# Kernel tuning notes

Hardware: AMD Instinct MI355X
Metric: run time of the kernel (lower is better)

Reference implementation:

```python
import jax, jax.numpy as jnp
import numpy as np

B, N_IN, N = 8, 256, 8192
D, K = 64, 512


def setup_inputs() -> dict:
    key = jax.random.key(0)
    k1, k2, k3 = jax.random.split(key, 3)
    z = jax.random.normal(k1, (B, N_IN, N), dtype=jnp.float32)
    W = jax.random.normal(k2, (D, N_IN), dtype=jnp.float32) * (1.0 / np.sqrt(N_IN))
    emb = jax.random.normal(k3, (K, D), dtype=jnp.float32)
    ind_hist = jnp.zeros((K,), dtype=jnp.float32)
    return {"z": z, "W": W, "emb": emb, "ind_hist": ind_hist}


def reference(z, W, emb, ind_hist):
    # 1x1 Conv1d, no bias: (B, n_in, N) x (d, n_in) -> (B, d, N)
    ze = jnp.einsum('bin,di->bdn', z, W)
    emb_sg = jax.lax.stop_gradient(emb)  # StopGrad on codebook

    # Squared L2 distance ze[b,:,n] vs emb[k,:], expanded identity to avoid (B,K,d,N)
    ze_sq = jnp.sum(ze * ze, axis=1)                      # (B, N)
    emb_sq = jnp.sum(emb_sg * emb_sg, axis=1)             # (K,)
    cross = jnp.einsum('bdn,kd->bkn', ze, emb_sg)         # (B, K, N)
    l2norm_sq = ze_sq[:, None, :] + emb_sq[None, :, None] - 2.0 * cross  # (B, K, N)

    ind = jnp.argmin(l2norm_sq, axis=1)                   # (B, N) nearest code per timestep
    zq = jnp.take(emb_sg, ind, axis=0).transpose(0, 2, 1)  # (B, d, N)

    # ReplaceGrad straight-through: forward value zq, gradient routed to ze
    zq_rg = ze + jax.lax.stop_gradient(zq - ze)

    # Scatter histogram of chosen indices, accumulated into ind_hist buffer
    counts = jax.ops.segment_sum(
        jnp.ones((B * N,), dtype=ind_hist.dtype), ind.reshape(-1), num_segments=K)
    new_hist = ind_hist + counts

    return zq_rg, new_hist
```

## Files before the change

### kernel.cpp

```cpp
#include <hip/hip_runtime.h>

#define B_SZ   8
#define NIN    256
#define NCOL   8192
#define DDIM   64
#define KCODES 512
#define ZQ_ELEMS (8ull * 64ull * 8192ull)

__global__ __launch_bounds__(256) void vq_prep(const float* __restrict__ W,
                                               const float* __restrict__ emb,
                                               const float* __restrict__ ind_hist,
                                               float* __restrict__ Wt,
                                               float* __restrict__ emb_sq,
                                               float* __restrict__ hist_out)
{
    int t = blockIdx.x * 256 + threadIdx.x;
    if (t < NIN * DDIM) {
        int i = t >> 6;
        int d = t & 63;
        Wt[t] = W[d * NIN + i];
    }
    if (t < KCODES) {
        const float* __restrict__ ek = emb + t * DDIM;
        float s = 0.f;
        #pragma unroll
        for (int d = 0; d < DDIM; ++d) s = fmaf(ek[d], ek[d], s);
        emb_sq[t] = s;
        hist_out[t] = ind_hist[t];
    }
}

__global__ __launch_bounds__(256, 4) void vq_main(const float* __restrict__ z,
                                                  const float* __restrict__ Wt,
                                                  const float* __restrict__ emb,
                                                  const float* __restrict__ emb_sq,
                                                  float* __restrict__ out,
                                                  float* __restrict__ hist)
{
    __shared__ float ze_lds[64][DDIM + 4];
    __shared__ float bw_lds[4][64];
    __shared__ int   bk_lds[4][64];

    const int tid = threadIdx.x;
    const int cl  = tid & 63;
    const int w   = __builtin_amdgcn_readfirstlane(tid >> 6);
    const int C   = blockIdx.x * 64 + cl;
    const int b   = C >> 13;
    const int n   = C & (NCOL - 1);

    {
        const float* __restrict__ zp = z + (size_t)b * NIN * NCOL + n;
        const float* __restrict__ wp = Wt + w * 16;

        float acc[16];
        #pragma unroll
        for (int j = 0; j < 16; ++j) acc[j] = 0.f;

        for (int i = 0; i < NIN; i += 2) {
            float z0 = zp[(size_t)(i + 0) * NCOL];
            float z1 = zp[(size_t)(i + 1) * NCOL];
            const float* __restrict__ w0 = wp + (size_t)i * DDIM;
            const float* __restrict__ w1 = w0 + DDIM;
            #pragma unroll
            for (int j = 0; j < 16; ++j) {
                float a = acc[j];
                a = fmaf(w0[j], z0, a);
                a = fmaf(w1[j], z1, a);
                acc[j] = a;
            }
        }
        #pragma unroll
        for (int j = 0; j < 16; ++j) ze_lds[cl][w * 16 + j] = acc[j];
    }
    __syncthreads();

    float ze[DDIM];
    #pragma unroll
    for (int j = 0; j < DDIM / 4; ++j) {
        float4 v = *reinterpret_cast<const float4*>(&ze_lds[cl][4 * j]);
        ze[4 * j + 0] = v.x;
        ze[4 * j + 1] = v.y;
        ze[4 * j + 2] = v.z;
        ze[4 * j + 3] = v.w;
    }

    float zesq = 0.f;
    #pragma unroll
    for (int d = 0; d < DDIM; ++d) zesq = fmaf(ze[d], ze[d], zesq);

    float best = 3.4e38f;
    int bestk = KCODES * w / 4;
    const int k0 = w * (KCODES / 4);
    for (int kk = 0; kk < KCODES / 4; ++kk) {
        const int k = k0 + kk;
        const float* __restrict__ ek = emb + (size_t)k * DDIM;
        float cr = 0.f;
        #pragma unroll
        for (int d = 0; d < DDIM; ++d) cr = fmaf(ek[d], ze[d], cr);
        float dist = (zesq + emb_sq[k]) - 2.0f * cr;
        if (dist < best) { best = dist; bestk = k; }
    }
    bw_lds[w][cl] = best;
    bk_lds[w][cl] = bestk;
    __syncthreads();

    float fb = bw_lds[0][cl];
    int   fk = bk_lds[0][cl];
    #pragma unroll
    for (int ww = 1; ww < 4; ++ww) {
        float v = bw_lds[ww][cl];
        int   kv = bk_lds[ww][cl];
        if (v < fb) { fb = v; fk = kv; }
    }

    if (w == 0) atomicAdd(hist + fk, 1.0f);

    const float4* __restrict__ eb =
        reinterpret_cast<const float4*>(emb + (size_t)fk * DDIM) + w * 4;
    float* __restrict__ op = out + ((size_t)b * DDIM + w * 16) * NCOL + n;
    #pragma unroll
    for (int v = 0; v < 4; ++v) {
        float4 e = eb[v];
        float z0 = ze_lds[cl][w * 16 + 4 * v + 0];
        float z1 = ze_lds[cl][w * 16 + 4 * v + 1];
        float z2 = ze_lds[cl][w * 16 + 4 * v + 2];
        float z3 = ze_lds[cl][w * 16 + 4 * v + 3];
        op[(size_t)(4 * v + 0) * NCOL] = z0 + (e.x - z0);
        op[(size_t)(4 * v + 1) * NCOL] = z1 + (e.y - z1);
        op[(size_t)(4 * v + 2) * NCOL] = z2 + (e.z - z2);
        op[(size_t)(4 * v + 3) * NCOL] = z3 + (e.w - z3);
    }
}

extern "C" void kernel_launch(void* const* d_in, const int* in_sizes, int n_in,
                              void* d_out, int out_size, void* d_ws, size_t ws_size,
                              hipStream_t stream)
{
    const float* z        = (const float*)d_in[0];
    const float* W        = (const float*)d_in[1];
    const float* emb      = (const float*)d_in[2];
    const float* ind_hist = (const float*)d_in[3];

    float* out  = (float*)d_out;
    float* hist = out + ZQ_ELEMS;

    float* Wt     = (float*)d_ws;
    float* emb_sq = Wt + NIN * DDIM;

    hipLaunchKernelGGL(vq_prep, dim3(64), dim3(256), 0, stream,
                       W, emb, ind_hist, Wt, emb_sq, hist);

    hipLaunchKernelGGL(vq_main, dim3(1024), dim3(256), 0, stream,
                       z, Wt, emb, emb_sq, out, hist);
}
```

Baseline: 134.2 us.

## Split fused VQ kernel into conv, split-K search, and finalize kernels

Splits the single fused kernel into three stages. The 1x1 conv writes ze to the output buffer. A codebook search runs on twice as many blocks, each covering half the codes, and merges results with 64-bit packed atomicMin on per-column candidates. A final kernel reads ze back, gathers the chosen code and updates the histogram. The aim is more parallelism and occupancy for the search, at the cost of extra global round-trips of ze, extra launches and atomics. The conv loop is also unrolled by 4 instead of 2.

```diff
diff --git a/kernel.cpp b/kernel.cpp
--- a/kernel.cpp
+++ b/kernel.cpp
@@ -1,10 +1,10 @@
 #include <hip/hip_runtime.h>
 
-#define B_SZ   8
 #define NIN    256
 #define NCOL   8192
 #define DDIM   64
 #define KCODES 512
+#define NCTOT  65536
 #define ZQ_ELEMS (8ull * 64ull * 8192ull)
 
 __global__ __launch_bounds__(256) void vq_prep(const float* __restrict__ W,
@@ -12,9 +12,11 @@
                                                const float* __restrict__ ind_hist,
                                                float* __restrict__ Wt,
                                                float* __restrict__ emb_sq,
+                                               unsigned long long* __restrict__ cand,
                                                float* __restrict__ hist_out)
 {
     int t = blockIdx.x * 256 + threadIdx.x;
+    cand[t] = ~0ull;
     if (t < NIN * DDIM) {
         int i = t >> 6;
         int d = t & 63;
@@ -30,17 +32,10 @@
     }
 }
 
-__global__ __launch_bounds__(256, 4) void vq_main(const float* __restrict__ z,
+__global__ __launch_bounds__(256, 4) void vq_conv(const float* __restrict__ z,
                                                   const float* __restrict__ Wt,
-                                                  const float* __restrict__ emb,
-                                                  const float* __restrict__ emb_sq,
-                                                  float* __restrict__ out,
-                                                  float* __restrict__ hist)
-{
-    __shared__ float ze_lds[64][DDIM + 4];
-    __shared__ float bw_lds[4][64];
-    __shared__ int   bk_lds[4][64];
-
+                                                  float* __restrict__ out)
+{
     const int tid = threadIdx.x;
     const int cl  = tid & 63;
     const int w   = __builtin_amdgcn_readfirstlane(tid >> 6);
@@ -48,50 +43,88 @@
     const int b   = C >> 13;
     const int n   = C & (NCOL - 1);
 
+    const float* __restrict__ zp = z + (size_t)b * NIN * NCOL + n;
+    const float* __restrict__ wp = Wt + w * 16;
+
+    float acc[16];
+    #pragma unroll
+    for (int j = 0; j < 16; ++j) acc[j] = 0.f;
+
+    for (int i = 0; i < NIN; i += 4) {
+        float z0 = zp[(size_t)(i + 0) * NCOL];
+        float z1 = zp[(size_t)(i + 1) * NCOL];
+        float z2 = zp[(size_t)(i + 2) * NCOL];
+        float z3 = zp[(size_t)(i + 3) * NCOL];
+        const float* __restrict__ w0 = wp + (size_t)(i + 0) * DDIM;
+        const float* __restrict__ w1 = wp + (size_t)(i + 1) * DDIM;
+        const float* __restrict__ w2 = wp + (size_t)(i + 2) * DDIM;
+        const float* __restrict__ w3 = wp + (size_t)(i + 3) * DDIM;
+        #pragma unroll
+        for (int j = 0; j < 16; ++j) {
+            float a = acc[j];
+            a = fmaf(w0[j], z0, a);
+            a = fmaf(w1[j], z1, a);
+            a = fmaf(w2[j], z2, a);
+            a = fmaf(w3[j], z3, a);
+            acc[j] = a;
+        }
+    }
+
+    float* __restrict__ op = out + ((size_t)b * DDIM + w * 16) * NCOL + n;
+    #pragma unroll
+    for (int j = 0; j < 16; ++j) op[(size_t)j * NCOL] = acc[j];
+}
+
+__global__ __launch_bounds__(256) void vq_search(const float* __restrict__ zeb,
+                                                 const float* __restrict__ emb,
+                                                 const float* __restrict__ emb_sq,
+                                                 unsigned long long* __restrict__ cand)
+{
+    __shared__ float ze_lds[64][DDIM + 4];
+
+    const int tid   = threadIdx.x;
+    const int C0    = (blockIdx.x >> 1) * 64;
+    const int khalf = blockIdx.x & 1;
+    const int b     = C0 >> 13;
+    const int n0    = C0 & (NCOL - 1);
+
     {
-        const float* __restrict__ zp = z + (size_t)b * NIN * NCOL + n;
-        const float* __restrict__ wp = Wt + w * 16;
-
-        float acc[16];
-        #pragma unroll
-        for (int j = 0; j < 16; ++j) acc[j] = 0.f;
-
-        for (int i = 0; i < NIN; i += 2) {
-            float z0 = zp[(size_t)(i + 0) * NCOL];
-            float z1 = zp[(size_t)(i + 1) * NCOL];
-            const float* __restrict__ w0 = wp + (size_t)i * DDIM;
-            const float* __restrict__ w1 = w0 + DDIM;
-            #pragma unroll
-            for (int j = 0; j < 16; ++j) {
-                float a = acc[j];
-                a = fmaf(w0[j], z0, a);
-                a = fmaf(w1[j], z1, a);
-                acc[j] = a;
-            }
+        const int r  = tid >> 2;
+        const int cc = (tid & 3) * 16;
+        const float4* __restrict__ src = reinterpret_cast<const float4*>(
+            zeb + ((size_t)b * DDIM + r) * NCOL + n0 + cc);
+        #pragma unroll
+        for (int v = 0; v < 4; ++v) {
+            float4 x = src[v];
+            ze_lds[cc + 4 * v + 0][r] = x.x;
+            ze_lds[cc + 4 * v + 1][r] = x.y;
+            ze_lds[cc + 4 * v + 2][r] = x.z;
+            ze_lds[cc + 4 * v + 3][r] = x.w;
         }
-        #pragma unroll
-        for (int j = 0; j < 16; ++j) ze_lds[cl][w * 16 + j] = acc[j];
     }
     __syncthreads();
 
+    const int lane = tid & 63;
+    const int w    = __builtin_amdgcn_readfirstlane(tid >> 6);
+
     float ze[DDIM];
     #pragma unroll
-    for (int j = 0; j < DDIM / 4; ++j) {
-        float4 v = *reinterpret_cast<const float4*>(&ze_lds[cl][4 * j]);
-        ze[4 * j + 0] = v.x;
-        ze[4 * j + 1] = v.y;
-        ze[4 * j + 2] = v.z;
-        ze[4 * j + 3] = v.w;
+    for (int q = 0; q < DDIM / 4; ++q) {
+        float4 v = *reinterpret_cast<const float4*>(&ze_lds[lane][4 * q]);
+        ze[4 * q + 0] = v.x;
+        ze[4 * q + 1] = v.y;
+        ze[4 * q + 2] = v.z;
+        ze[4 * q + 3] = v.w;
     }
 
     float zesq = 0.f;
     #pragma unroll
     for (int d = 0; d < DDIM; ++d) zesq = fmaf(ze[d], ze[d], zesq);
 
-    float best = 3.4e38f;
-    int bestk = KCODES * w / 4;
-    const int k0 = w * (KCODES / 4);
-    for (int kk = 0; kk < KCODES / 4; ++kk) {
+    const int k0 = khalf * (KCODES / 2) + w * 64;
+    float best  = 3.4e38f;
+    int   bestk = k0;
+    for (int kk = 0; kk < 64; ++kk) {
         const int k = k0 + kk;
         const float* __restrict__ ek = emb + (size_t)k * DDIM;
         float cr = 0.f;
@@ -100,19 +133,48 @@
         float dist = (zesq + emb_sq[k]) - 2.0f * cr;
         if (dist < best) { best = dist; bestk = k; }
     }
-    bw_lds[w][cl] = best;
-    bk_lds[w][cl] = bestk;
+
+    unsigned u   = __float_as_uint(best);
+    unsigned enc = u ^ ((unsigned)((int)u >> 31) | 0x80000000u);
+    unsigned long long pk =
+        ((unsigned long long)enc << 32) | (unsigned)bestk;
+    atomicMin(&cand[C0 + lane], pk);
+}
+
+__global__ __launch_bounds__(256, 4) void vq_final(const float* __restrict__ emb,
+                                                   const unsigned long long* __restrict__ cand,
+                                                   float* __restrict__ out,
+                                                   float* __restrict__ hist)
+{
+    __shared__ float ze_lds[64][DDIM + 4];
+
+    const int tid = threadIdx.x;
+    const int C0  = blockIdx.x * 64;
+    const int b   = C0 >> 13;
+    const int n0  = C0 & (NCOL - 1);
+
+    {
+        const int r  = tid >> 2;
+        const int cc = (tid & 3) * 16;
+        const float4* __restrict__ src = reinterpret_cast<const float4*>(
+            out + ((size_t)b * DDIM + r) * NCOL + n0 + cc);
+        #pragma unroll
+        for (int v = 0; v < 4; ++v) {
+            float4 x = src[v];
+            ze_lds[cc + 4 * v + 0][r] = x.x;
+            ze_lds[cc + 4 * v + 1][r] = x.y;
+            ze_lds[cc + 4 * v + 2][r] = x.z;
+            ze_lds[cc + 4 * v + 3][r] = x.w;
+        }
+    }
     __syncthreads();
 
-    float fb = bw_lds[0][cl];
-    int   fk = bk_lds[0][cl];
-    #pragma unroll
-    for (int ww = 1; ww < 4; ++ww) {
-        float v = bw_lds[ww][cl];
-        int   kv = bk_lds[ww][cl];
-        if (v < fb) { fb = v; fk = kv; }
-    }
-
+    const int lane = tid & 63;
+    const int w    = __builtin_amdgcn_readfirstlane(tid >> 6);
+    const int C    = C0 + lane;
+    const int n    = n0 + lane;
+
+    const int fk = (int)(unsigned)cand[C];
     if (w == 0) atomicAdd(hist + fk, 1.0f);
 
     const float4* __restrict__ eb =
@@ -121,10 +183,10 @@
     #pragma unroll
     for (int v = 0; v < 4; ++v) {
         float4 e = eb[v];
-        float z0 = ze_lds[cl][w * 16 + 4 * v + 0];
-        float z1 = ze_lds[cl][w * 16 + 4 * v + 1];
-        float z2 = ze_lds[cl][w * 16 + 4 * v + 2];
-        float z3 = ze_lds[cl][w * 16 + 4 * v + 3];
+        float z0 = ze_lds[lane][w * 16 + 4 * v + 0];
+        float z1 = ze_lds[lane][w * 16 + 4 * v + 1];
+        float z2 = ze_lds[lane][w * 16 + 4 * v + 2];
+        float z3 = ze_lds[lane][w * 16 + 4 * v + 3];
         op[(size_t)(4 * v + 0) * NCOL] = z0 + (e.x - z0);
         op[(size_t)(4 * v + 1) * NCOL] = z1 + (e.y - z1);
         op[(size_t)(4 * v + 2) * NCOL] = z2 + (e.z - z2);
@@ -144,12 +206,19 @@
     float* out  = (float*)d_out;
     float* hist = out + ZQ_ELEMS;
 
-    float* Wt     = (float*)d_ws;
+    unsigned long long* cand = (unsigned long long*)d_ws;
+    float* Wt     = (float*)((char*)d_ws + NCTOT * 8);
     float* emb_sq = Wt + NIN * DDIM;
 
-    hipLaunchKernelGGL(vq_prep, dim3(64), dim3(256), 0, stream,
-                       W, emb, ind_hist, Wt, emb_sq, hist);
-
-    hipLaunchKernelGGL(vq_main, dim3(1024), dim3(256), 0, stream,
-                       z, Wt, emb, emb_sq, out, hist);
-}
+    hipLaunchKernelGGL(vq_prep, dim3(NCTOT / 256), dim3(256), 0, stream,
+                       W, emb, ind_hist, Wt, emb_sq, cand, hist);
+
+    hipLaunchKernelGGL(vq_conv, dim3(1024), dim3(256), 0, stream,
+                       z, Wt, out);
+
+    hipLaunchKernelGGL(vq_search, dim3(2048), dim3(256), 0, stream,
+                       out, emb, emb_sq, cand);
+
+    hipLaunchKernelGGL(vq_final, dim3(1024), dim3(256), 0, stream,
+                       emb, cand, out, hist);
+}
```

Measured after the change: 170.3 us. +26.9%, slower.

## Transpose codebook and tile distance search over 32 codes per pass

Applied to the files above, without the earlier changes.

Adds a transposed codebook (embT) built in the prep kernel, and restructures the distance search so each thread keeps 32 running dot products and streams ze from LDS one dimension at a time. This replaces keeping 64 ze values in registers with keeping 32 accumulators. The codebook reads stay wave-uniform, so they can go through scalar loads. It also unrolls the projection loop by 4 and pads the LDS rows by 1 to avoid bank conflicts. The cost is more LDS reads for ze and a larger workspace.

```diff
diff --git a/kernel.cpp b/kernel.cpp
--- a/kernel.cpp
+++ b/kernel.cpp
@@ -1,6 +1,5 @@
 #include <hip/hip_runtime.h>
 
-#define B_SZ   8
 #define NIN    256
 #define NCOL   8192
 #define DDIM   64
@@ -11,14 +10,20 @@
                                                const float* __restrict__ emb,
                                                const float* __restrict__ ind_hist,
                                                float* __restrict__ Wt,
+                                               float* __restrict__ embT,
                                                float* __restrict__ emb_sq,
                                                float* __restrict__ hist_out)
 {
-    int t = blockIdx.x * 256 + threadIdx.x;
+    const int t = blockIdx.x * 256 + threadIdx.x;
     if (t < NIN * DDIM) {
         int i = t >> 6;
         int d = t & 63;
         Wt[t] = W[d * NIN + i];
+    }
+    {
+        int d = t >> 9;
+        int k = t & 511;
+        embT[t] = emb[k * DDIM + d];
     }
     if (t < KCODES) {
         const float* __restrict__ ek = emb + t * DDIM;
@@ -33,11 +38,12 @@
 __global__ __launch_bounds__(256, 4) void vq_main(const float* __restrict__ z,
                                                   const float* __restrict__ Wt,
                                                   const float* __restrict__ emb,
+                                                  const float* __restrict__ embT,
                                                   const float* __restrict__ emb_sq,
                                                   float* __restrict__ out,
                                                   float* __restrict__ hist)
 {
-    __shared__ float ze_lds[64][DDIM + 4];
+    __shared__ float ze_lds[64][DDIM + 1];
     __shared__ float bw_lds[4][64];
     __shared__ int   bk_lds[4][64];
 
@@ -56,16 +62,22 @@
         #pragma unroll
         for (int j = 0; j < 16; ++j) acc[j] = 0.f;
 
-        for (int i = 0; i < NIN; i += 2) {
+        for (int i = 0; i < NIN; i += 4) {
             float z0 = zp[(size_t)(i + 0) * NCOL];
             float z1 = zp[(size_t)(i + 1) * NCOL];
-            const float* __restrict__ w0 = wp + (size_t)i * DDIM;
-            const float* __restrict__ w1 = w0 + DDIM;
+            float z2 = zp[(size_t)(i + 2) * NCOL];
+            float z3 = zp[(size_t)(i + 3) * NCOL];
+            const float* __restrict__ w0 = wp + (size_t)(i + 0) * DDIM;
+            const float* __restrict__ w1 = wp + (size_t)(i + 1) * DDIM;
+            const float* __restrict__ w2 = wp + (size_t)(i + 2) * DDIM;
+            const float* __restrict__ w3 = wp + (size_t)(i + 3) * DDIM;
             #pragma unroll
             for (int j = 0; j < 16; ++j) {
                 float a = acc[j];
                 a = fmaf(w0[j], z0, a);
                 a = fmaf(w1[j], z1, a);
+                a = fmaf(w2[j], z2, a);
+                a = fmaf(w3[j], z3, a);
                 acc[j] = a;
             }
         }
@@ -74,31 +86,40 @@
     }
     __syncthreads();
 
-    float ze[DDIM];
-    #pragma unroll
-    for (int j = 0; j < DDIM / 4; ++j) {
-        float4 v = *reinterpret_cast<const float4*>(&ze_lds[cl][4 * j]);
-        ze[4 * j + 0] = v.x;
-        ze[4 * j + 1] = v.y;
-        ze[4 * j + 2] = v.z;
-        ze[4 * j + 3] = v.w;
+    float zesq = 0.f;
+    #pragma unroll 4
+    for (int d = 0; d < DDIM; ++d) {
+        float zd = ze_lds[cl][d];
+        zesq = fmaf(zd, zd, zesq);
     }
 
-    float zesq = 0.f;
-    #pragma unroll
-    for (int d = 0; d < DDIM; ++d) zesq = fmaf(ze[d], ze[d], zesq);
+    const int k0 = w * (KCODES / 4);
+    float best  = 3.4e38f;
+    int   bestk = k0;
 
-    float best = 3.4e38f;
-    int bestk = KCODES * w / 4;
-    const int k0 = w * (KCODES / 4);
-    for (int kk = 0; kk < KCODES / 4; ++kk) {
-        const int k = k0 + kk;
-        const float* __restrict__ ek = emb + (size_t)k * DDIM;
-        float cr = 0.f;
+    for (int t4 = 0; t4 < 4; ++t4) {
+        const int kt = k0 + t4 * 32;
+        const float* __restrict__ ep0 = embT + kt;
+
+        float acc[32];
         #pragma unroll
-        for (int d = 0; d < DDIM; ++d) cr = fmaf(ek[d], ze[d], cr);
-        float dist = (zesq + emb_sq[k]) - 2.0f * cr;
-        if (dist < best) { best = dist; bestk = k; }
+        for (int kk = 0; kk < 32; ++kk) acc[kk] = 0.f;
+
+        #pragma unroll 2
+        for (int d = 0; d < DDIM; ++d) {
+            float zd = ze_lds[cl][d];
+            const float* __restrict__ ep = ep0 + (size_t)d * KCODES;
+            #pragma unroll
+            for (int kk = 0; kk < 32; ++kk)
+                acc[kk] = fmaf(ep[kk], zd, acc[kk]);
+        }
+
+        #pragma unroll
+        for (int kk = 0; kk < 32; ++kk) {
+            const int k = kt + kk;
+            float dist = (zesq + emb_sq[k]) - 2.0f * acc[kk];
+            if (dist < best) { best = dist; bestk = k; }
+        }
     }
     bw_lds[w][cl] = best;
     bk_lds[w][cl] = bestk;
@@ -109,7 +130,7 @@
     #pragma unroll
     for (int ww = 1; ww < 4; ++ww) {
         float v = bw_lds[ww][cl];
-        int   kv = bk_lds[ww][cl];
+        int  kv = bk_lds[ww][cl];
         if (v < fb) { fb = v; fk = kv; }
     }
 
@@ -145,11 +166,12 @@
     float* hist = out + ZQ_ELEMS;
 
     float* Wt     = (float*)d_ws;
-    float* emb_sq = Wt + NIN * DDIM;
+    float* embT   = Wt + NIN * DDIM;
+    float* emb_sq = embT + DDIM * KCODES;
 
-    hipLaunchKernelGGL(vq_prep, dim3(64), dim3(256), 0, stream,
-                       W, emb, ind_hist, Wt, emb_sq, hist);
+    hipLaunchKernelGGL(vq_prep, dim3(128), dim3(256), 0, stream,
+                       W, emb, ind_hist, Wt, embT, emb_sq, hist);
 
     hipLaunchKernelGGL(vq_main, dim3(1024), dim3(256), 0, stream,
-                       z, Wt, emb, emb_sq, out, hist);
+                       z, Wt, emb, embT, emb_sq, out, hist);
 }
```

After: 123.8 us, median of 2. 7.8% less time.
